# Kernel tuning notes

Hardware: AMD Instinct MI355X
Metric: run time of the kernel (lower is better)

The kernel has to match this reference:

```python
import jax, jax.numpy as jnp
import numpy as np

D_MODEL = 2048
N_HEADS = 16
N_KV = 8
HEAD_DIM = 128
G = N_HEADS // N_KV  # q heads per kv head
SCALE = float(np.sqrt(HEAD_DIM))
B, T = 2, 2048


def setup_inputs() -> dict:
    key = jax.random.key(0)
    k1, k2, k3, k4, k5 = jax.random.split(key, 5)
    s = 0.02
    return {
        "x": jax.random.normal(k1, (B, T, D_MODEL), dtype=jnp.float32),
        "Wq": jax.random.normal(k2, (N_HEADS * HEAD_DIM, D_MODEL), dtype=jnp.float32) * s,
        "Wk": jax.random.normal(k3, (N_KV * HEAD_DIM, D_MODEL), dtype=jnp.float32) * s,
        "Wv": jax.random.normal(k4, (N_KV * HEAD_DIM, D_MODEL), dtype=jnp.float32) * s,
        "Wo": jax.random.normal(k5, (D_MODEL, N_HEADS * HEAD_DIM), dtype=jnp.float32) * s,
    }


def reference(x, Wq, Wk, Wv, Wo):
    # Projections (nn.Linear: y = x @ W.T), dropout prob = 0 so omitted.
    b, t, _ = x.shape
    q = (x @ Wq.T).reshape(b, t, N_KV, G, HEAD_DIM)   # (B,T,Hkv,G,d)
    k = (x @ Wk.T).reshape(b, t, N_KV, HEAD_DIM)      # (B,T,Hkv,d)
    v = (x @ Wv.T).reshape(b, t, N_KV, HEAD_DIM)
    # GQA: each kv head shared by G query heads (equivalent to repeat_interleave).
    scores = jnp.einsum('btghd,bsgd->bghts', q, k) / SCALE  # (B,Hkv,G,T,T)
    attn = jax.nn.softmax(scores, axis=-1)
    out = jnp.einsum('bghts,bsgd->btghd', attn, v)          # (B,T,Hkv,G,d)
    out = out.reshape(b, t, N_HEADS * HEAD_DIM)
    return out @ Wo.T
```

## Files before the change

### kernel.cpp

```cpp
#include <hip/hip_runtime.h>
#include <hip/hip_bf16.h>

typedef __attribute__((ext_vector_type(8))) short short8;
typedef __attribute__((ext_vector_type(4))) float floatx4;

__device__ inline unsigned short f2bf(float f) {
    unsigned int u = __float_as_uint(f);
    u += 0x7fffu + ((u >> 16) & 1u);
    return (unsigned short)(u >> 16);
}

__device__ inline unsigned int pk_bf16(float lo, float hi) {
    __hip_bfloat162 h = __float22bfloat162_rn(float2{lo, hi});
    unsigned int u;
    __builtin_memcpy(&u, &h, 4);
    return u;
}

__global__ void cast_all_kernel(const float* __restrict__ x,
                                const float* __restrict__ wq,
                                const float* __restrict__ wk,
                                const float* __restrict__ wv,
                                const float* __restrict__ wo,
                                unsigned short* __restrict__ xb,
                                unsigned short* __restrict__ wqkb,
                                unsigned short* __restrict__ wvb,
                                unsigned short* __restrict__ wob) {
    const float C2 = 0.08838834764831845f * 1.4426950408889634f;
    int bid = blockIdx.x;
    const float* src;
    unsigned short* dst;
    int base;
    float sc = 1.0f;
    if (bid < 8192)       { src = x;  dst = xb;             base = bid; }
    else if (bid < 12288) { src = wq; dst = wqkb;           base = bid - 8192; sc = C2; }
    else if (bid < 14336) { src = wk; dst = wqkb + 4194304; base = bid - 12288; }
    else if (bid < 16384) { src = wv; dst = wvb;            base = bid - 14336; }
    else                  { src = wo; dst = wob;            base = bid - 16384; }
    int i = base * 256 + threadIdx.x;
    float4 v = ((const float4*)src)[i];
    ushort4 o;
    o.x = f2bf(v.x * sc); o.y = f2bf(v.y * sc);
    o.z = f2bf(v.z * sc); o.w = f2bf(v.w * sc);
    ((ushort4*)dst)[i] = o;
}

template <int OUT_BF16>
__device__ __forceinline__ void gemm_bt64_body(
        const unsigned short* __restrict__ A,
        const unsigned short* __restrict__ B,
        void* __restrict__ Cp, int K, int ldc, int m0, int n0,
        unsigned short* sA, unsigned short* sB) {
    const int tid  = threadIdx.x;
    const int wave = tid >> 6;
    const int lane = tid & 63;
    const int l16  = lane & 15;
    const int lq   = lane >> 4;
    const int wm   = (wave >> 1) * 64;
    const int wn   = (wave & 1) * 64;

    floatx4 acc[4][4] = {};

    const unsigned short* gA[4];
    const unsigned short* gB[4];
#pragma unroll
    for (int i = 0; i < 4; i++) {
        int c   = wave * 4 + i;
        int row = c * 8 + (lane >> 3);
        int chs = (lane & 7) ^ (row & 7);
        gA[i] = A + (size_t)(m0 + row) * K + chs * 8;
        gB[i] = B + (size_t)(n0 + row) * K + chs * 8;
    }

    for (int k0 = 0; k0 < K; k0 += 64) {
        __syncthreads();
#pragma unroll
        for (int i = 0; i < 4; i++) {
            int c = wave * 4 + i;
            __builtin_amdgcn_global_load_lds(
                (const __attribute__((address_space(1))) void*)gA[i],
                (__attribute__((address_space(3))) void*)(sA + c * 512), 16, 0, 0);
            gA[i] += 64;
            __builtin_amdgcn_global_load_lds(
                (const __attribute__((address_space(1))) void*)gB[i],
                (__attribute__((address_space(3))) void*)(sB + c * 512), 16, 0, 0);
            gB[i] += 64;
        }
        __syncthreads();

        short8 af[2][4], bfr[2][4];
#pragma unroll
        for (int ks = 0; ks < 2; ks++) {
            int slot = (ks * 4 + lq) ^ (l16 & 7);
#pragma unroll
            for (int mb = 0; mb < 4; mb++)
                af[ks][mb] = *(const short8*)(sA + (wm + mb * 16 + l16) * 64 + slot * 8);
#pragma unroll
            for (int nb = 0; nb < 4; nb++)
                bfr[ks][nb] = *(const short8*)(sB + (wn + nb * 16 + l16) * 64 + slot * 8);
        }
#pragma unroll
        for (int ks = 0; ks < 2; ks++)
#pragma unroll
            for (int mb = 0; mb < 4; mb++)
#pragma unroll
                for (int nb = 0; nb < 4; nb++)
                    acc[mb][nb] = __builtin_amdgcn_mfma_f32_16x16x32_bf16(
                        af[ks][mb], bfr[ks][nb], acc[mb][nb], 0, 0, 0);
    }

#pragma unroll
    for (int mb = 0; mb < 4; mb++)
#pragma unroll
        for (int nb = 0; nb < 4; nb++)
#pragma unroll
            for (int r = 0; r < 4; r++) {
                int row = m0 + wm + mb * 16 + lq * 4 + r;
                int col = n0 + wn + nb * 16 + l16;
                if (OUT_BF16)
                    ((unsigned short*)Cp)[(size_t)row * ldc + col] = f2bf(acc[mb][nb][r]);
                else
                    ((float*)Cp)[(size_t)row * ldc + col] = acc[mb][nb][r];
            }
}

__global__ __launch_bounds__(256) void gemm_qkv_kernel(
        const unsigned short* __restrict__ x_bf,
        const unsigned short* __restrict__ Wqk,
        const unsigned short* __restrict__ Wv,
        unsigned short* __restrict__ QKb,
        unsigned short* __restrict__ Vtb) {
    __shared__ __align__(16) unsigned short sA[128 * 64];
    __shared__ __align__(16) unsigned short sB[128 * 64];
    const int bid = blockIdx.x;
    if (bid < 768) {
        gemm_bt64_body<1>(x_bf, Wqk, QKb, 2048, 3072,
                          (bid / 24) * 128, (bid % 24) * 128, sA, sB);
    } else {
        int t = bid - 768;
        gemm_bt64_body<1>(Wv, x_bf, Vtb, 2048, 4096,
                          (t / 32) * 128, (t % 32) * 128, sA, sB);
    }
}

__global__ __launch_bounds__(256) void gemm_o_kernel(
        const unsigned short* __restrict__ A,
        const unsigned short* __restrict__ B,
        float* __restrict__ C) {
    __shared__ __align__(16) unsigned short sA[128 * 64];
    __shared__ __align__(16) unsigned short sB[128 * 64];
    gemm_bt64_body<0>(A, B, C, 2048, 2048,
                      blockIdx.y * 128, blockIdx.x * 128, sA, sB);
}

__global__ __launch_bounds__(256, 2) void flash_kernel(
        const unsigned short* __restrict__ QK,
        const unsigned short* __restrict__ Vt,
        unsigned short* __restrict__ O) {
    __shared__ __align__(16) unsigned short smem[40960];

    const int tid  = threadIdx.x;
    const int wave = tid >> 6;
    const int lane = tid & 63;
    const int l16  = lane & 15;
    const int lq   = lane >> 4;
    const int wq   = wave >> 1;
    const int wk   = wave & 1;
    const int qt   = blockIdx.x;
    const int bh   = blockIdx.y;
    const int b    = bh >> 4;
    const int h    = bh & 15;
    const int kvh  = h >> 1;
    const size_t tokbase = (size_t)b * 2048 + qt * 128 + wq * 64;

    short8 qf[4][4];
#pragma unroll
    for (int qb = 0; qb < 4; qb++) {
        const unsigned short* qp =
            QK + (tokbase + qb * 16 + l16) * 3072 + h * 128 + lq * 8;
#pragma unroll
        for (int c = 0; c < 4; c++) qf[qb][c] = *(const short8*)(qp + c * 32);
    }

    const unsigned short* gKe =
        QK + ((size_t)b * 2048 + wave * 16 + lq) * 3072 + 2048 + kvh * 128 +
        (l16 ^ lq) * 8;
    const unsigned short* gKo =
        QK + ((size_t)b * 2048 + wave * 16 + 4 + lq) * 3072 + 2048 + kvh * 128 +
        (l16 ^ (lq + 4)) * 8;
    const unsigned short* gV0 =
        Vt + (size_t)(kvh * 128 + wave * 32 + (lane >> 3)) * 4096 +
        (size_t)b * 2048 + ((lane & 7) ^ (lane >> 3)) * 8;

#define STAGE_KT(sKd, sVd)                                                     \
    do {                                                                       \
        _Pragma("unroll")                                                      \
        for (int i = 0; i < 4; i++) {                                          \
            const unsigned short* gk =                                         \
                ((i & 1) ? gKo : gKe) + (i >> 1) * 24576;                      \
            __builtin_amdgcn_global_load_lds(                                  \
                (const __attribute__((address_space(1))) void*)gk,             \
                (__attribute__((address_space(3))) void*)((sKd) +              \
                                                          (wave * 4 + i) * 512),\
                16, 0, 0);                                                     \
            __builtin_amdgcn_global_load_lds(                                  \
                (const __attribute__((address_space(1))) void*)(gV0 +          \
                                                               i * 32768),     \
                (__attribute__((address_space(3))) void*)((sVd) +              \
                                                          (wave * 4 + i) * 512),\
                16, 0, 0);                                                     \
        }                                                                      \
        gKe += 196608; gKo += 196608; gV0 += 64;                               \
    } while (0)

    unsigned short* pB = smem + 32768 + wq * 4096;

    floatx4 oacc[4][8] = {};
    float l_run[4] = {0.0f, 0.0f, 0.0f, 0.0f};

    STAGE_KT(smem, smem + 16384);
    asm volatile("s_waitcnt vmcnt(0)" ::: "memory");
    __builtin_amdgcn_s_barrier();
    asm volatile("" ::: "memory");

    for (int kt = 0; kt < 32; kt++) {
        const int cur = kt & 1;
        unsigned short* sKc = smem + cur * 8192;
        unsigned short* sVc = smem + 16384 + cur * 8192;
        if (kt < 31) {
            unsigned short* sKn = smem + (cur ^ 1) * 8192;
            unsigned short* sVn = smem + 16384 + (cur ^ 1) * 8192;
            STAGE_KT(sKn, sVn);
        }

#pragma unroll
        for (int kb = 0; kb < 2; kb++) {
            floatx4 sacc[4] = {};
#pragma unroll
            for (int c = 0; c < 4; c++) {
                short8 kf = *(const short8*)(
                    sKc + (wk * 32 + kb * 16 + l16) * 128 +
                    (((c * 4 + lq) ^ (l16 & 7)) * 8));
#pragma unroll
                for (int qb = 0; qb < 4; qb++)
                    sacc[qb] = __builtin_amdgcn_mfma_f32_16x16x32_bf16(
                        kf, qf[qb][c], sacc[qb], 0, 0, 0);
            }
#pragma unroll
            for (int qb = 0; qb < 4; qb++) {
                float p0 = __builtin_exp2f(sacc[qb][0]);
                float p1 = __builtin_exp2f(sacc[qb][1]);
                float p2 = __builtin_exp2f(sacc[qb][2]);
                float p3 = __builtin_exp2f(sacc[qb][3]);
                l_run[qb] += (p0 + p1) + (p2 + p3);
                int row = qb * 16 + l16;
                uint2 u;
                u.x = pk_bf16(p0, p1);
                u.y = pk_bf16(p2, p3);
                *(uint2*)(pB + row * 64 +
                          (((wk * 4 + kb * 2 + (lq >> 1)) ^ (row & 7)) * 8) +
                          (lq & 1) * 4) = u;
            }
        }
        asm volatile("s_waitcnt lgkmcnt(0)" ::: "memory");

        short8 pf[4];
#pragma unroll
        for (int qb = 0; qb < 4; qb++) {
            int row = qb * 16 + l16;
            pf[qb] = *(const short8*)(pB + row * 64 +
                                      (((wk * 4 + lq) ^ (row & 7)) * 8));
        }
#pragma unroll
        for (int nb = 0; nb < 8; nb++) {
            short8 vf = *(const short8*)(
                sVc + (nb * 16 + l16) * 64 +
                (((wk * 4 + lq) ^ (l16 & 7)) * 8));
#pragma unroll
            for (int qb = 0; qb < 4; qb++)
                oacc[qb][nb] = __builtin_amdgcn_mfma_f32_16x16x32_bf16(
                    vf, pf[qb], oacc[qb][nb], 0, 0, 0);
        }

        asm volatile("s_waitcnt vmcnt(0)" ::: "memory");
        __builtin_amdgcn_s_barrier();
        asm volatile("" ::: "memory");
    }
#undef STAGE_KT

    __syncthreads();
#pragma unroll
    for (int qb = 0; qb < 4; qb++) {
        float l = l_run[qb];
        l += __shfl_xor(l, 16);
        l += __shfl_xor(l, 32);
        l_run[qb] = l;
    }
    float* red  = (float*)smem;
    float* lred = (float*)(smem + 33792);
    if (wk) {
#pragma unroll
        for (int qb = 0; qb < 4; qb++) {
            lred[wq * 64 + qb * 16 + l16] = l_run[qb];
#pragma unroll
            for (int nb = 0; nb < 8; nb++)
                *(floatx4*)(red + wq * 8448 + (qb * 16 + l16) * 132 +
                            nb * 16 + lq * 4) = oacc[qb][nb];
        }
    }
    __syncthreads();
    if (!wk) {
#pragma unroll
        for (int qb = 0; qb < 4; qb++) {
            float inv = 1.0f / (l_run[qb] + lred[wq * 64 + qb * 16 + l16]);
            size_t row = (tokbase + qb * 16 + l16) * 2048 + h * 128;
#pragma unroll
            for (int nb = 0; nb < 8; nb++) {
                floatx4 o2 = *(const floatx4*)(red + wq * 8448 +
                                               (qb * 16 + l16) * 132 +
                                               nb * 16 + lq * 4);
                uint2 u;
                u.x = pk_bf16((oacc[qb][nb][0] + o2[0]) * inv,
                              (oacc[qb][nb][1] + o2[1]) * inv);
                u.y = pk_bf16((oacc[qb][nb][2] + o2[2]) * inv,
                              (oacc[qb][nb][3] + o2[3]) * inv);
                *(uint2*)(O + row + nb * 16 + lq * 4) = u;
            }
        }
    }
}

extern "C" void kernel_launch(void* const* d_in, const int* in_sizes, int n_in,
                              void* d_out, int out_size, void* d_ws, size_t ws_size,
                              hipStream_t stream) {
    const float* x  = (const float*)d_in[0];
    const float* Wq = (const float*)d_in[1];
    const float* Wk = (const float*)d_in[2];
    const float* Wv = (const float*)d_in[3];
    const float* Wo = (const float*)d_in[4];

    char* ws = (char*)d_ws;
    unsigned short* x_bf   = (unsigned short*)(ws);
    unsigned short* Wqk_bf = (unsigned short*)(ws + 16777216);
    unsigned short* Wv_bf  = (unsigned short*)(ws + 29360128);
    unsigned short* Wo_bf  = (unsigned short*)(ws + 33554432);
    unsigned short* QKb    = (unsigned short*)(ws + 41943040);
    unsigned short* Vtb    = (unsigned short*)(ws + 67108864);
    unsigned short* Ob     = (unsigned short*)(ws + 75497472);

    cast_all_kernel<<<dim3(20480), 256, 0, stream>>>(
        x, Wq, Wk, Wv, Wo, x_bf, Wqk_bf, Wv_bf, Wo_bf);

    gemm_qkv_kernel<<<dim3(1024), 256, 0, stream>>>(x_bf, Wqk_bf, Wv_bf, QKb, Vtb);

    flash_kernel<<<dim3(16, 32), 256, 0, stream>>>(QKb, Vtb, Ob);

    gemm_o_kernel<<<dim3(16, 32), 256, 0, stream>>>(Ob, Wo_bf, (float*)d_out);
}
```

Before: 329.7 us.

## Split flash attention waves by query rows instead of key halves

```diff
diff --git a/kernel.cpp b/kernel.cpp
--- a/kernel.cpp
+++ b/kernel.cpp
@@ -164,18 +164,16 @@
     const int lane = tid & 63;
     const int l16  = lane & 15;
     const int lq   = lane >> 4;
-    const int wq   = wave >> 1;
-    const int wk   = wave & 1;
     const int qt   = blockIdx.x;
     const int bh   = blockIdx.y;
     const int b    = bh >> 4;
     const int h    = bh & 15;
     const int kvh  = h >> 1;
-    const size_t tokbase = (size_t)b * 2048 + qt * 128 + wq * 64;
-
-    short8 qf[4][4];
-#pragma unroll
-    for (int qb = 0; qb < 4; qb++) {
+    const size_t tokbase = (size_t)b * 2048 + qt * 128 + wave * 32;
+
+    short8 qf[2][4];
+#pragma unroll
+    for (int qb = 0; qb < 2; qb++) {
         const unsigned short* qp =
             QK + (tokbase + qb * 16 + l16) * 3072 + h * 128 + lq * 8;
 #pragma unroll
@@ -213,10 +211,10 @@
         gKe += 196608; gKo += 196608; gV0 += 64;                               \
     } while (0)
 
-    unsigned short* pB = smem + 32768 + wq * 4096;
-
-    floatx4 oacc[4][8] = {};
-    float l_run[4] = {0.0f, 0.0f, 0.0f, 0.0f};
+    unsigned short* pB = smem + 32768 + wave * 2048;
+
+    floatx4 oacc[2][8] = {};
+    float l_run[2] = {0.0f, 0.0f};
 
     STAGE_KT(smem, smem + 16384);
     asm volatile("s_waitcnt vmcnt(0)" ::: "memory");
@@ -225,8 +223,8 @@
 
     for (int kt = 0; kt < 32; kt++) {
         const int cur = kt & 1;
-        unsigned short* sKc = smem + cur * 8192;
-        unsigned short* sVc = smem + 16384 + cur * 8192;
+        const unsigned short* sKc = smem + cur * 8192;
+        const unsigned short* sVc = smem + 16384 + cur * 8192;
         if (kt < 31) {
             unsigned short* sKn = smem + (cur ^ 1) * 8192;
             unsigned short* sVn = smem + 16384 + (cur ^ 1) * 8192;
@@ -235,19 +233,18 @@
 
 #pragma unroll
         for (int kb = 0; kb < 2; kb++) {
-            floatx4 sacc[4] = {};
+            floatx4 sacc[2] = {};
 #pragma unroll
             for (int c = 0; c < 4; c++) {
                 short8 kf = *(const short8*)(
-                    sKc + (wk * 32 + kb * 16 + l16) * 128 +
-                    (((c * 4 + lq) ^ (l16 & 7)) * 8));
-#pragma unroll
-                for (int qb = 0; qb < 4; qb++)
+                    sKc + (kb * 16 + l16) * 128 + (((c * 4 + lq) ^ (l16 & 7)) * 8));
+#pragma unroll
+                for (int qb = 0; qb < 2; qb++)
                     sacc[qb] = __builtin_amdgcn_mfma_f32_16x16x32_bf16(
                         kf, qf[qb][c], sacc[qb], 0, 0, 0);
             }
 #pragma unroll
-            for (int qb = 0; qb < 4; qb++) {
+            for (int qb = 0; qb < 2; qb++) {
                 float p0 = __builtin_exp2f(sacc[qb][0]);
                 float p1 = __builtin_exp2f(sacc[qb][1]);
                 float p2 = __builtin_exp2f(sacc[qb][2]);
@@ -258,29 +255,81 @@
                 u.x = pk_bf16(p0, p1);
                 u.y = pk_bf16(p2, p3);
                 *(uint2*)(pB + row * 64 +
-                          (((wk * 4 + kb * 2 + (lq >> 1)) ^ (row & 7)) * 8) +
+                          (((kb * 2 + (lq >> 1)) ^ (row & 7)) * 8) +
                           (lq & 1) * 4) = u;
             }
         }
         asm volatile("s_waitcnt lgkmcnt(0)" ::: "memory");
 
-        short8 pf[4];
-#pragma unroll
-        for (int qb = 0; qb < 4; qb++) {
+        short8 pf0[2];
+#pragma unroll
+        for (int qb = 0; qb < 2; qb++) {
             int row = qb * 16 + l16;
-            pf[qb] = *(const short8*)(pB + row * 64 +
-                                      (((wk * 4 + lq) ^ (row & 7)) * 8));
-        }
+            pf0[qb] = *(const short8*)(pB + row * 64 +
+                                       ((lq ^ (row & 7)) * 8));
+        }
+
+        __builtin_amdgcn_s_setprio(1);
 #pragma unroll
         for (int nb = 0; nb < 8; nb++) {
             short8 vf = *(const short8*)(
-                sVc + (nb * 16 + l16) * 64 +
-                (((wk * 4 + lq) ^ (l16 & 7)) * 8));
-#pragma unroll
-            for (int qb = 0; qb < 4; qb++)
+                sVc + (nb * 16 + l16) * 64 + ((lq ^ (l16 & 7)) * 8));
+#pragma unroll
+            for (int qb = 0; qb < 2; qb++)
                 oacc[qb][nb] = __builtin_amdgcn_mfma_f32_16x16x32_bf16(
-                    vf, pf[qb], oacc[qb][nb], 0, 0, 0);
-        }
+                    vf, pf0[qb], oacc[qb][nb], 0, 0, 0);
+        }
+        __builtin_amdgcn_s_setprio(0);
+
+#pragma unroll
+        for (int kb = 2; kb < 4; kb++) {
+            floatx4 sacc[2] = {};
+#pragma unroll
+            for (int c = 0; c < 4; c++) {
+                short8 kf = *(const short8*)(
+                    sKc + (kb * 16 + l16) * 128 + (((c * 4 + lq) ^ (l16 & 7)) * 8));
+#pragma unroll
+                for (int qb = 0; qb < 2; qb++)
+                    sacc[qb] = __builtin_amdgcn_mfma_f32_16x16x32_bf16(
+                        kf, qf[qb][c], sacc[qb], 0, 0, 0);
+            }
+#pragma unroll
+            for (int qb = 0; qb < 2; qb++) {
+                float p0 = __builtin_exp2f(sacc[qb][0]);
+                float p1 = __builtin_exp2f(sacc[qb][1]);
+                float p2 = __builtin_exp2f(sacc[qb][2]);
+                float p3 = __builtin_exp2f(sacc[qb][3]);
+                l_run[qb] += (p0 + p1) + (p2 + p3);
+                int row = qb * 16 + l16;
+                uint2 u;
+                u.x = pk_bf16(p0, p1);
+                u.y = pk_bf16(p2, p3);
+                *(uint2*)(pB + row * 64 +
+                          (((kb * 2 + (lq >> 1)) ^ (row & 7)) * 8) +
+                          (lq & 1) * 4) = u;
+            }
+        }
+        asm volatile("s_waitcnt lgkmcnt(0)" ::: "memory");
+
+        short8 pf1[2];
+#pragma unroll
+        for (int qb = 0; qb < 2; qb++) {
+            int row = qb * 16 + l16;
+            pf1[qb] = *(const short8*)(pB + row * 64 +
+                                       (((4 + lq) ^ (row & 7)) * 8));
+        }
+
+        __builtin_amdgcn_s_setprio(1);
+#pragma unroll
+        for (int nb = 0; nb < 8; nb++) {
+            short8 vf = *(const short8*)(
+                sVc + (nb * 16 + l16) * 64 + (((4 + lq) ^ (l16 & 7)) * 8));
+#pragma unroll
+            for (int qb = 0; qb < 2; qb++)
+                oacc[qb][nb] = __builtin_amdgcn_mfma_f32_16x16x32_bf16(
+                    vf, pf1[qb], oacc[qb][nb], 0, 0, 0);
+        }
+        __builtin_amdgcn_s_setprio(0);
 
         asm volatile("s_waitcnt vmcnt(0)" ::: "memory");
         __builtin_amdgcn_s_barrier();
@@ -288,44 +337,19 @@
     }
 #undef STAGE_KT
 
-    __syncthreads();
-#pragma unroll
-    for (int qb = 0; qb < 4; qb++) {
+#pragma unroll
+    for (int qb = 0; qb < 2; qb++) {
         float l = l_run[qb];
         l += __shfl_xor(l, 16);
         l += __shfl_xor(l, 32);
-        l_run[qb] = l;
-    }
-    float* red  = (float*)smem;
-    float* lred = (float*)(smem + 33792);
-    if (wk) {
-#pragma unroll
-        for (int qb = 0; qb < 4; qb++) {
-            lred[wq * 64 + qb * 16 + l16] = l_run[qb];
-#pragma unroll
-            for (int nb = 0; nb < 8; nb++)
-                *(floatx4*)(red + wq * 8448 + (qb * 16 + l16) * 132 +
-                            nb * 16 + lq * 4) = oacc[qb][nb];
-        }
-    }
-    __syncthreads();
-    if (!wk) {
-#pragma unroll
-        for (int qb = 0; qb < 4; qb++) {
-            float inv = 1.0f / (l_run[qb] + lred[wq * 64 + qb * 16 + l16]);
-            size_t row = (tokbase + qb * 16 + l16) * 2048 + h * 128;
-#pragma unroll
-            for (int nb = 0; nb < 8; nb++) {
-                floatx4 o2 = *(const floatx4*)(red + wq * 8448 +
-                                               (qb * 16 + l16) * 132 +
-                                               nb * 16 + lq * 4);
-                uint2 u;
-                u.x = pk_bf16((oacc[qb][nb][0] + o2[0]) * inv,
-                              (oacc[qb][nb][1] + o2[1]) * inv);
-                u.y = pk_bf16((oacc[qb][nb][2] + o2[2]) * inv,
-                              (oacc[qb][nb][3] + o2[3]) * inv);
-                *(uint2*)(O + row + nb * 16 + lq * 4) = u;
-            }
+        float inv = 1.0f / l;
+        size_t row = (tokbase + qb * 16 + l16) * 2048 + h * 128;
+#pragma unroll
+        for (int nb = 0; nb < 8; nb++) {
+            uint2 u;
+            u.x = pk_bf16(oacc[qb][nb][0] * inv, oacc[qb][nb][1] * inv);
+            u.y = pk_bf16(oacc[qb][nb][2] * inv, oacc[qb][nb][3] * inv);
+            *(uint2*)(O + row + nb * 16 + lq * 4) = u;
         }
     }
 }
```

Result: no change. 326.6 us (-0.9%).
